# Kernel tuning notes

Hardware: AMD Instinct MI355X
Metric: run time of the kernel (lower is better)

The kernel has to match this reference:

```python
import jax, jax.numpy as jnp
import numpy as np
from functools import partial

H = 512          # hidden_size
H4 = H // 4      # goal hidden size
ENC = 8          # enc_steps
DEC = 12         # dec_steps
PRED = 2         # pred_dim (ETH)
B = 512          # batch


def _lin(k, i, o, s=0.05):
    kw, kb = jax.random.split(k)
    return jax.random.normal(kw, (i, o), jnp.float32) * s, jax.random.normal(kb, (o,), jnp.float32) * s


def setup_inputs() -> dict:
    key = jax.random.key(0)
    ks = jax.random.split(key, 32)
    d = {"inputs": jax.random.normal(ks[0], (B, ENC, 6), jnp.float32)}
    d["embed_w"], d["embed_b"] = _lin(ks[1], 6, H)
    d["reg_w"], d["reg_b"] = _lin(ks[2], H, PRED)
    d["ea_w"], d["ea_b"] = _lin(ks[3], H4, 1)
    d["da_w"], d["da_b"] = _lin(ks[4], H4, 1)
    d["e2g_w"], d["e2g_b"] = _lin(ks[5], H, H4)
    d["e2d_w"], d["e2d_b"] = _lin(ks[6], H, H)
    d["gh2i_w"], d["gh2i_b"] = _lin(ks[7], H4, H4)
    d["dh2i_w"], d["dh2i_b"] = _lin(ks[8], H, H)
    d["gh2t_w"], d["gh2t_b"] = _lin(ks[9], H4, H)
    d["g2e_w"], d["g2e_b"] = _lin(ks[10], H4, H4)
    d["g2d_w"], d["g2d_b"] = _lin(ks[11], H4, H4)
    d["enc_wih"], _ = _lin(ks[12], H + H4, 3 * H)
    d["enc_whh"], _ = _lin(ks[13], H, 3 * H)
    d["enc_bih"] = jax.random.normal(ks[14], (3 * H,), jnp.float32) * 0.05
    d["enc_bhh"] = jax.random.normal(ks[15], (3 * H,), jnp.float32) * 0.05
    d["goal_wih"], _ = _lin(ks[16], H4, 3 * H4)
    d["goal_whh"], _ = _lin(ks[17], H4, 3 * H4)
    d["goal_bih"] = jax.random.normal(ks[18], (3 * H4,), jnp.float32) * 0.05
    d["goal_bhh"] = jax.random.normal(ks[19], (3 * H4,), jnp.float32) * 0.05
    d["dec_wih"], _ = _lin(ks[20], H + H4, 3 * H)
    d["dec_whh"], _ = _lin(ks[21], H, 3 * H)
    d["dec_bih"] = jax.random.normal(ks[22], (3 * H,), jnp.float32) * 0.05
    d["dec_bhh"] = jax.random.normal(ks[23], (3 * H,), jnp.float32) * 0.05
    return d


def _gru(x, h, wih, whh, bih, bhh):
    gi = x @ wih + bih          # [B, 3H]
    gh = h @ whh + bhh
    ir, iz, inn = jnp.split(gi, 3, axis=-1)
    hr, hz, hn = jnp.split(gh, 3, axis=-1)
    r = jax.nn.sigmoid(ir + hr)
    z = jax.nn.sigmoid(iz + hz)
    n = jnp.tanh(inn + r * hn)
    return (1.0 - z) * n + z * h


def reference(inputs, embed_w, embed_b, reg_w, reg_b, ea_w, ea_b, da_w, da_b,
              e2g_w, e2g_b, e2d_w, e2d_b, gh2i_w, gh2i_b, dh2i_w, dh2i_b,
              gh2t_w, gh2t_b, g2e_w, g2e_b, g2d_w, g2d_b,
              enc_wih, enc_whh, enc_bih, enc_bhh,
              goal_wih, goal_whh, goal_bih, goal_bhh,
              dec_wih, dec_whh, dec_bih, dec_bhh):
    relu = jax.nn.relu
    b = inputs.shape[0]
    traj_input = relu(inputs @ embed_w + embed_b)           # [B, ENC, H]

    def sge(goal_hidden):
        def gstep(carry, _):
            gh, gi = carry
            gh = _gru(gi, gh, goal_wih, goal_whh, goal_bih, goal_bhh)
            gi = relu(gh @ gh2i_w + gh2i_b)
            return (gh, gi), gh
        gi0 = jnp.zeros((b, H4), traj_input.dtype)
        _, goals = jax.lax.scan(gstep, (goal_hidden, gi0), None, length=DEC)  # [DEC,B,H4]
        goal_traj = relu(goals @ gh2t_w + gh2t_b) @ reg_w + reg_b             # [DEC,B,PRED]
        goal_for_dec = relu(goals @ g2d_w + g2d_b)                            # [DEC,B,H4]
        gfe = relu(goals @ g2e_w + g2e_b).transpose(1, 0, 2)                  # [B,DEC,H4]
        logits = relu(jnp.tanh(gfe) @ ea_w + ea_b)[..., 0]                    # [B,DEC]
        attn = jax.nn.softmax(logits, axis=1)
        goal_for_enc = jnp.einsum('bt,bth->bh', attn, gfe)
        return goal_for_dec, goal_for_enc, goal_traj.transpose(1, 0, 2)

    def decoder(dec_hidden, gfd):
        gfd_b = gfd.transpose(1, 0, 2)  # [B,DEC,H4]
        steps = jnp.arange(DEC)
        def dstep(dh, t):
            mask = (steps >= t)[None, :, None]
            gdi = jnp.where(mask, gfd_b, 0.0)                      # zeros before t, faithful to torch
            logits = relu(jnp.tanh(gdi) @ da_w + da_b)[..., 0]     # [B,DEC]
            attn = jax.nn.softmax(logits, axis=1)
            ctx = jnp.einsum('bt,bth->bh', attn, gdi)
            ddi = relu(dh @ dh2i_w + dh2i_b)
            x = jnp.concatenate([ctx, ddi], axis=-1)
            dh = _gru(x, dh, dec_wih, dec_whh, dec_bih, dec_bhh)
            return dh, dh @ reg_w + reg_b
        _, traj = jax.lax.scan(dstep, dec_hidden, steps)           # [DEC,B,PRED]
        return traj.transpose(1, 0, 2)

    def estep(carry, x_t):
        teh, gfe = carry
        teh = _gru(jnp.concatenate([x_t, gfe], axis=1), teh,
                   enc_wih, enc_whh, enc_bih, enc_bhh)
        goal_hidden = relu(teh @ e2g_w + e2g_b)
        dec_hidden = relu(teh @ e2d_w + e2d_b)
        gfd, gfe, goal_traj = sge(goal_hidden)
        dec_traj = decoder(dec_hidden, gfd)
        return (teh, gfe), (goal_traj, dec_traj)

    teh0 = jnp.zeros((b, H), traj_input.dtype)
    gfe0 = jnp.zeros((b, H4), traj_input.dtype)
    _, (all_goal, all_dec) = jax.lax.scan(estep, (teh0, gfe0),
                                          traj_input.transpose(1, 0, 2))
    # [ENC,B,DEC,PRED] -> [B,ENC,DEC,PRED]
    return all_goal.transpose(1, 0, 2, 3), all_dec.transpose(1, 0, 2, 3)
```

## Files before the change

### kernel.cpp

```cpp
#include <hip/hip_runtime.h>


typedef unsigned short u16;
typedef __attribute__((ext_vector_type(8))) short bf16x8;
typedef __attribute__((ext_vector_type(4))) float f32x4;

static __device__ __forceinline__ float b2f(u16 u) {
  union { float f; unsigned int i; } x; x.i = ((unsigned int)u) << 16; return x.f;
}
static __device__ __forceinline__ u16 f2b(float f) {
  unsigned int u = __float_as_uint(f);
  unsigned int r = (u + 0x7FFFu + ((u >> 16) & 1u)) >> 16;
  return (u16)r;
}
static __device__ __forceinline__ float fsig(float x) {
  return __fdividef(1.f, 1.f + __expf(-x));
}
static __device__ __forceinline__ float ftanh(float x) {
  return 1.f - __fdividef(2.f, __expf(2.f * x) + 1.f);
}

struct TransArgs {
  const float* in[13];
  u16* out[13];
  int K[13], N[13], t0[13], nx[13];
};

__global__ __launch_bounds__(256) void transpose_all(TransArgs ta) {
  int bid = blockIdx.x;
  int i = 0;
  for (int k = 1; k < 13; k++) if (bid >= ta.t0[k]) i = k;
  const float* in = ta.in[i];
  u16* out = ta.out[i];
  int K = ta.K[i], N = ta.N[i];
  int local = bid - ta.t0[i];
  int nx = ta.nx[i];
  int tx = local % nx, ty = local / nx;
  __shared__ u16 tbuf[32][33];
  int n0 = tx * 32, k0 = ty * 32;
  int x = threadIdx.x & 31, y = threadIdx.x >> 5;
  for (int q = 0; q < 4; q++) tbuf[y + 8 * q][x] = f2b(in[(size_t)(k0 + y + 8 * q) * N + n0 + x]);
  __syncthreads();
  for (int q = 0; q < 4; q++) out[(size_t)(n0 + y + 8 * q) * K + k0 + x] = tbuf[x][y + 8 * q];
}

__global__ __launch_bounds__(256) void embed_kernel(const float* __restrict__ inp,
                                                    const float* __restrict__ w,
                                                    const float* __restrict__ bias,
                                                    u16* __restrict__ traj) {
  int t = blockIdx.x * 256 + threadIdx.x;
  int h = t & 511, b = (t >> 9) & 511, e = t >> 18;
  float acc = bias[h];
  for (int i = 0; i < 6; i++) acc += inp[(b * 8 + e) * 6 + i] * w[i * 512 + h];
  traj[((e * 512) + b) * 512 + h] = f2b(fmaxf(acc, 0.f));
}

struct GDesc {
  const u16* A; int lda;
  const u16* A2; int lda2; int asplit;
  const u16* W; int ldw;
  const float* bias;
  u16* Cb; int ldc;
  float* Cf;
  u16* Cb2; int ldc2; int route_n;
  int K; int relu; int nblk; int mblk;
};

__global__ __launch_bounds__(256) void gemm128(GDesc d0, GDesc d1) {
  GDesc d = (blockIdx.z == 0) ? d0 : d1;
  if ((int)blockIdx.x >= d.nblk || (int)blockIdx.y >= d.mblk) return;
  __shared__ u16 As[128][72];
  __shared__ u16 Bs[128][72];
  int tid = threadIdx.x;
  int m0 = blockIdx.y * 128, n0 = blockIdx.x * 128;
  int lane = tid & 63, wave = tid >> 6;
  int wr = wave >> 1, wc = wave & 1;
  int mrow = lane & 15, kq = (lane >> 4) * 8;
  int srow = tid >> 3, scol = (tid & 7) * 8;
  f32x4 acc[4][4] = {};

  for (int k0 = 0; k0 < d.K; k0 += 64) {
    const u16* Asrc; int Alda, kk;
    if (k0 < d.asplit) { Asrc = d.A; Alda = d.lda; kk = k0; }
    else               { Asrc = d.A2; Alda = d.lda2; kk = k0 - d.asplit; }
    __syncthreads();
#pragma unroll
    for (int p = 0; p < 4; p++) {
      int r = srow + p * 32;
      *(uint4*)&As[r][scol] = *(const uint4*)&Asrc[(size_t)(m0 + r) * Alda + kk + scol];
      *(uint4*)&Bs[r][scol] = *(const uint4*)&d.W[(size_t)(n0 + r) * d.ldw + k0 + scol];
    }
    __syncthreads();
#pragma unroll
    for (int ks = 0; ks < 2; ks++) {
      bf16x8 af[4], bf[4];
#pragma unroll
      for (int i = 0; i < 4; i++) {
        af[i] = *(const bf16x8*)&As[wr * 64 + i * 16 + mrow][ks * 32 + kq];
        bf[i] = *(const bf16x8*)&Bs[wc * 64 + i * 16 + mrow][ks * 32 + kq];
      }
#pragma unroll
      for (int i = 0; i < 4; i++)
#pragma unroll
        for (int j = 0; j < 4; j++)
          acc[i][j] = __builtin_amdgcn_mfma_f32_16x16x32_bf16(af[i], bf[j], acc[i][j], 0, 0, 0);
    }
  }
  int col = lane & 15, rq = (lane >> 4) * 4;
#pragma unroll
  for (int j = 0; j < 4; j++) {
    int n = n0 + wc * 64 + j * 16 + col;
    float bv = d.bias ? d.bias[n] : 0.f;
    bool r2 = (n >= d.route_n);
    u16* cb = r2 ? d.Cb2 : d.Cb;
    int ldc = r2 ? d.ldc2 : d.ldc;
    int nn = r2 ? n - d.route_n : n;
#pragma unroll
    for (int i = 0; i < 4; i++)
#pragma unroll
      for (int r = 0; r < 4; r++) {
        int m = m0 + wr * 64 + i * 16 + rq + r;
        float v = acc[i][j][r] + bv;
        if (d.relu) v = fmaxf(v, 0.f);
        cb[(size_t)m * ldc + nn] = f2b(v);
        if (d.Cf) d.Cf[(size_t)m * d.ldc + n] = v;
      }
  }
}

__global__ __launch_bounds__(256) void head_reg(const u16* __restrict__ goals,
                                                const u16* __restrict__ w_t,
                                                const float* __restrict__ wb,
                                                const float* __restrict__ rw,
                                                const float* __restrict__ rb,
                                                float* __restrict__ out) {
  int tid = threadIdx.x;
  int lane = tid & 63, wave = tid >> 6;
  int rbase = (blockIdx.x * 4 + wave) * 64;
  int mrow = lane & 15, kq = (lane >> 4) * 8;
  int col = lane & 15, rq4 = (lane >> 4) * 4;
  bf16x8 a[4][4];
#pragma unroll
  for (int q = 0; q < 4; q++)
#pragma unroll
    for (int ks = 0; ks < 4; ks++)
      a[q][ks] = *(const bf16x8*)&goals[(size_t)(rbase + q * 16 + mrow) * 128 + ks * 32 + kq];
  float pr0[4][4] = {}, pr1[4][4] = {};
  for (int j = 0; j < 32; j++) {
    bf16x8 b[4];
#pragma unroll
    for (int ks = 0; ks < 4; ks++)
      b[ks] = *(const bf16x8*)&w_t[(size_t)(j * 16 + mrow) * 128 + ks * 32 + kq];
    f32x4 acc[4] = {};
#pragma unroll
    for (int ks = 0; ks < 4; ks++)
#pragma unroll
      for (int q = 0; q < 4; q++)
        acc[q] = __builtin_amdgcn_mfma_f32_16x16x32_bf16(a[q][ks], b[ks], acc[q], 0, 0, 0);
    int n = j * 16 + col;
    float bv = wb[n];
    float rw0 = rw[n * 2], rw1 = rw[n * 2 + 1];
#pragma unroll
    for (int q = 0; q < 4; q++)
#pragma unroll
      for (int r = 0; r < 4; r++) {
        float v = fmaxf(acc[q][r] + bv, 0.f);
        pr0[q][r] += v * rw0;
        pr1[q][r] += v * rw1;
      }
  }
#pragma unroll
  for (int q = 0; q < 4; q++)
#pragma unroll
    for (int r = 0; r < 4; r++)
#pragma unroll
      for (int o = 1; o < 16; o <<= 1) {
        pr0[q][r] += __shfl_xor(pr0[q][r], o);
        pr1[q][r] += __shfl_xor(pr1[q][r], o);
      }
  if (col == 0) {
#pragma unroll
    for (int q = 0; q < 4; q++)
#pragma unroll
      for (int r = 0; r < 4; r++) {
        int m = rbase + q * 16 + rq4 + r;
        int e = m / 6144; int rem = m - e * 6144;
        int t = rem >> 9; int b = rem & 511;
        float* o = out + ((size_t)(b * 8 + e) * 12 + t) * 2;
        o[0] = pr0[q][r] + rb[0];
        o[1] = pr1[q][r] + rb[1];
      }
  }
}

__global__ __launch_bounds__(1024) void gru_dh2i_reg(const u16* __restrict__ gi,
                                                     const u16* __restrict__ gh,
                                                     float* __restrict__ hf,
                                                     u16* __restrict__ hb,
                                                     const u16* __restrict__ w_t,
                                                     const float* __restrict__ wb,
                                                     u16* __restrict__ ddi,
                                                     const float* __restrict__ rw,
                                                     const float* __restrict__ rb,
                                                     float* __restrict__ out, int td) {
  __shared__ u16 dhs[16][520];
  __shared__ u16 dds[16][520];
  int tid = threadIdx.x;
  int lane = tid & 63, wave = tid >> 6;
  int r0 = blockIdx.x * 16;
  {
    int r = r0 + wave;
    int j8 = lane * 8;
    size_t base = (size_t)r * 1536 + j8;
    uint4 ir4 = *(const uint4*)&gi[base];
    uint4 iz4 = *(const uint4*)&gi[base + 512];
    uint4 in4 = *(const uint4*)&gi[base + 1024];
    uint4 hr4 = *(const uint4*)&gh[base];
    uint4 hz4 = *(const uint4*)&gh[base + 512];
    uint4 hn4 = *(const uint4*)&gh[base + 1024];
    const u16* irp = (const u16*)&ir4; const u16* izp = (const u16*)&iz4;
    const u16* inp = (const u16*)&in4; const u16* hrp = (const u16*)&hr4;
    const u16* hzp = (const u16*)&hz4; const u16* hnp = (const u16*)&hn4;
    size_t hoff = (size_t)r * 512 + j8;
    float hv[8];
    *(float4*)&hv[0] = *(const float4*)&hf[hoff];
    *(float4*)&hv[4] = *(const float4*)&hf[hoff + 4];
    u16 hbv[8];
    float p0 = 0.f, p1 = 0.f;
    for (int j = 0; j < 8; j++) {
      float rr = fsig(b2f(irp[j]) + b2f(hrp[j]));
      float zz = fsig(b2f(izp[j]) + b2f(hzp[j]));
      float nn = ftanh(b2f(inp[j]) + rr * b2f(hnp[j]));
      float ho = (1.f - zz) * nn + zz * hv[j];
      hv[j] = ho; hbv[j] = f2b(ho);
      p0 += ho * rw[(j8 + j) * 2];
      p1 += ho * rw[(j8 + j) * 2 + 1];
    }
    *(float4*)&hf[hoff] = *(const float4*)&hv[0];
    *(float4*)&hf[hoff + 4] = *(const float4*)&hv[4];
    *(uint4*)&hb[hoff] = *(const uint4*)&hbv[0];
    *(uint4*)&dhs[wave][j8] = *(const uint4*)&hbv[0];
    for (int o = 32; o; o >>= 1) { p0 += __shfl_down(p0, o); p1 += __shfl_down(p1, o); }
    if (lane == 0) {
      int e = r >> 9, b = r & 511;
      size_t off = ((size_t)(b * 8 + e) * 12 + td) * 2;
      out[off] = p0 + rb[0];
      out[off + 1] = p1 + rb[1];
    }
  }
  __syncthreads();
  int mrow = lane & 15, kq = (lane >> 4) * 8, rq4 = (lane >> 4) * 4;
#pragma unroll
  for (int q = 0; q < 2; q++) {
    int n0 = (wave * 2 + q) * 16;
    f32x4 acc = {};
#pragma unroll
    for (int ks = 0; ks < 16; ks++) {
      bf16x8 a = *(const bf16x8*)&dhs[mrow][ks * 32 + kq];
      bf16x8 bfr = *(const bf16x8*)&w_t[(size_t)(n0 + mrow) * 512 + ks * 32 + kq];
      acc = __builtin_amdgcn_mfma_f32_16x16x32_bf16(a, bfr, acc, 0, 0, 0);
    }
    float bv = wb[n0 + mrow];
#pragma unroll
    for (int x = 0; x < 4; x++)
      dds[rq4 + x][n0 + mrow] = f2b(fmaxf(acc[x] + bv, 0.f));
  }
  __syncthreads();
  int rr = tid >> 6, c8 = (tid & 63) * 8;
  *(uint4*)&ddi[(size_t)(r0 + rr) * 512 + c8] = *(const uint4*)&dds[rr][c8];
}

__global__ __launch_bounds__(1024) void goal_mega(const u16* __restrict__ gi_g,
                                                  const u16* __restrict__ gh_g,
                                                  float* __restrict__ teh_f,
                                                  u16* __restrict__ teh_out,
                                                  const u16* __restrict__ e2g_t,
                                                  const float* __restrict__ e2g_b,
                                                  const u16* __restrict__ wih_t,
                                                  const u16* __restrict__ whh_t,
                                                  const float* __restrict__ bih,
                                                  const float* __restrict__ bhh,
                                                  const u16* __restrict__ g2i_t,
                                                  const float* __restrict__ g2i_b,
                                                  const u16* __restrict__ g2e_t,
                                                  const float* __restrict__ g2e_b,
                                                  const float* __restrict__ eaw,
                                                  const float* __restrict__ eab,
                                                  u16* __restrict__ goals,
                                                  u16* __restrict__ gfe_out) {
  __shared__ float ghf[16][128];
  __shared__ u16   ghb[16][136];
  __shared__ u16   gib[16][136];
  __shared__ float gi3[16][388];
  __shared__ float gh3[16][388];
  __shared__ u16   gfe_l[12][16][128];
  __shared__ u16   tehb[16][520];
  int tid = threadIdx.x;
  int r0 = blockIdx.x * 16;
  int lane = tid & 63, wave = tid >> 6;
  int mrow = lane & 15, kq = (lane >> 4) * 8;
  int rq4 = (lane >> 4) * 4;

  bool isI = (wave < 8);
  int tbase = isI ? wave : wave - 8;
  bf16x8 Bf[3][4];
  float  bias1[3];
  int    n0s[3];
#pragma unroll
  for (int i = 0; i < 3; i++) {
    int n0 = (tbase + 8 * i) * 16;
    n0s[i] = n0;
    const u16* Wt = isI ? wih_t : whh_t;
#pragma unroll
    for (int ks = 0; ks < 4; ks++)
      Bf[i][ks] = *(const bf16x8*)&Wt[(n0 + mrow) * 128 + ks * 32 + kq];
    bias1[i] = (isI ? bih : bhh)[n0 + mrow];
  }
  bf16x8 Gf[4];
  float bias3;
  {
    const u16* W3 = isI ? g2i_t : g2e_t;
    const float* B3 = isI ? g2i_b : g2e_b;
    int n0 = (wave & 7) * 16;
#pragma unroll
    for (int ks = 0; ks < 4; ks++)
      Gf[ks] = *(const bf16x8*)&W3[(n0 + mrow) * 128 + ks * 32 + kq];
    bias3 = B3[n0 + mrow];
  }

  {
    u16* gz = &gib[0][0];
    for (int idx = tid; idx < 16 * 136; idx += 1024) gz[idx] = 0;
  }

  {
    int r = wave;
    int j8 = lane * 8;
    int grow = r0 + r;
    size_t base = (size_t)grow * 1536 + j8;
    uint4 ir4 = *(const uint4*)&gi_g[base];
    uint4 iz4 = *(const uint4*)&gi_g[base + 512];
    uint4 in4 = *(const uint4*)&gi_g[base + 1024];
    uint4 hr4 = *(const uint4*)&gh_g[base];
    uint4 hz4 = *(const uint4*)&gh_g[base + 512];
    uint4 hn4 = *(const uint4*)&gh_g[base + 1024];
    const u16* irp = (const u16*)&ir4; const u16* izp = (const u16*)&iz4;
    const u16* inp = (const u16*)&in4; const u16* hrp = (const u16*)&hr4;
    const u16* hzp = (const u16*)&hz4; const u16* hnp = (const u16*)&hn4;
    size_t hoff = (size_t)grow * 512 + j8;
    float hv[8];
    *(float4*)&hv[0] = *(const float4*)&teh_f[hoff];
    *(float4*)&hv[4] = *(const float4*)&teh_f[hoff + 4];
    u16 hbv[8];
    for (int j = 0; j < 8; j++) {
      float rr = fsig(b2f(irp[j]) + b2f(hrp[j]));
      float zz = fsig(b2f(izp[j]) + b2f(hzp[j]));
      float nn = ftanh(b2f(inp[j]) + rr * b2f(hnp[j]));
      float ho = (1.f - zz) * nn + zz * hv[j];
      hv[j] = ho; hbv[j] = f2b(ho);
    }
    *(float4*)&teh_f[hoff] = *(const float4*)&hv[0];
    *(float4*)&teh_f[hoff + 4] = *(const float4*)&hv[4];
    *(uint4*)&teh_out[hoff] = *(const uint4*)&hbv[0];
    *(uint4*)&tehb[r][j8] = *(const uint4*)&hbv[0];
  }
  __syncthreads();

  if (wave < 8) {
    int n0 = wave * 16;
    f32x4 acc = {};
#pragma unroll
    for (int ks = 0; ks < 16; ks++) {
      bf16x8 a = *(const bf16x8*)&tehb[mrow][ks * 32 + kq];
      bf16x8 b = *(const bf16x8*)&e2g_t[(size_t)(n0 + mrow) * 512 + ks * 32 + kq];
      acc = __builtin_amdgcn_mfma_f32_16x16x32_bf16(a, b, acc, 0, 0, 0);
    }
    int n = n0 + mrow;
    float bv = e2g_b[n];
#pragma unroll
    for (int r = 0; r < 4; r++) {
      float v = fmaxf(acc[r] + bv, 0.f);
      int m = rq4 + r;
      ghf[m][n] = v;
      ghb[m][n] = f2b(v);
    }
  }
  __syncthreads();

  for (int t = 0; t < 12; t++) {
    bf16x8 ag[4];
#pragma unroll
    for (int ks = 0; ks < 4; ks++)
      ag[ks] = isI ? *(const bf16x8*)&gib[mrow][ks * 32 + kq]
                   : *(const bf16x8*)&ghb[mrow][ks * 32 + kq];
    float* G = isI ? &gi3[0][0] : &gh3[0][0];
#pragma unroll
    for (int i = 0; i < 3; i++) {
      f32x4 acc = {};
#pragma unroll
      for (int ks = 0; ks < 4; ks++)
        acc = __builtin_amdgcn_mfma_f32_16x16x32_bf16(ag[ks], Bf[i][ks], acc, 0, 0, 0);
      int n = n0s[i] + mrow;
#pragma unroll
      for (int r = 0; r < 4; r++)
        G[(rq4 + r) * 388 + n] = acc[r] + bias1[i];
    }
    __syncthreads();
    for (int idx = tid; idx < 2048; idx += 1024) {
      int m = idx >> 7, j = idx & 127;
      float rr = fsig(gi3[m][j] + gh3[m][j]);
      float zz = fsig(gi3[m][128 + j] + gh3[m][128 + j]);
      float nn = ftanh(gi3[m][256 + j] + rr * gh3[m][256 + j]);
      float h = ghf[m][j];
      float ho = (1.f - zz) * nn + zz * h;
      ghf[m][j] = ho;
      ghb[m][j] = f2b(ho);
    }
    __syncthreads();
    if (wave < 4) {
      int idx = wave * 64 + lane;
      int row = idx >> 4, c8 = (idx & 15) * 8;
      uint4 v = *(const uint4*)&ghb[row][c8];
      *(uint4*)&goals[(size_t)(t * 512 + r0 + row) * 128 + c8] = v;
    }
    {
      f32x4 acc = {};
#pragma unroll
      for (int ks = 0; ks < 4; ks++) {
        bf16x8 a = *(const bf16x8*)&ghb[mrow][ks * 32 + kq];
        acc = __builtin_amdgcn_mfma_f32_16x16x32_bf16(a, Gf[ks], acc, 0, 0, 0);
      }
      int n = (wave & 7) * 16 + mrow;
      if (isI) {
#pragma unroll
        for (int r = 0; r < 4; r++)
          gib[rq4 + r][n] = f2b(fmaxf(acc[r] + bias3, 0.f));
      } else {
#pragma unroll
        for (int r = 0; r < 4; r++)
          gfe_l[t][rq4 + r][n] = f2b(fmaxf(acc[r] + bias3, 0.f));
      }
    }
    __syncthreads();
  }

  {
    int m = wave;
    float w0 = eaw[lane], w1 = eaw[lane + 64];
    float eb = eab[0];
    float v0[12], v1[12], lg[12];
#pragma unroll
    for (int t = 0; t < 12; t++) {
      float a = b2f(gfe_l[t][m][lane]);
      float c = b2f(gfe_l[t][m][lane + 64]);
      v0[t] = a; v1[t] = c;
      float p = ftanh(a) * w0 + ftanh(c) * w1;
      for (int o = 32; o; o >>= 1) p += __shfl_xor(p, o);
      lg[t] = fmaxf(p + eb, 0.f);
    }
    float mx = lg[0];
#pragma unroll
    for (int t = 1; t < 12; t++) mx = fmaxf(mx, lg[t]);
    float s = 0.f;
#pragma unroll
    for (int t = 0; t < 12; t++) { lg[t] = __expf(lg[t] - mx); s += lg[t]; }
    float inv = __fdividef(1.f, s);
    float c0 = 0.f, c1 = 0.f;
#pragma unroll
    for (int t = 0; t < 12; t++) { c0 += lg[t] * inv * v0[t]; c1 += lg[t] * inv * v1[t]; }
    gfe_out[(r0 + m) * 128 + lane] = f2b(c0);
    gfe_out[(r0 + m) * 128 + lane + 64] = f2b(c1);
  }
}

__global__ __launch_bounds__(256) void attn_ctx_all(const u16* __restrict__ gfd,
                                                    const float* __restrict__ daw,
                                                    const float* __restrict__ dab,
                                                    u16* __restrict__ xctx) {
  int row = (blockIdx.x * 256 + threadIdx.x) >> 6;
  int lane = threadIdx.x & 63;
  int e = row >> 9, b = row & 511;
  float w0 = daw[lane], w1 = daw[lane + 64];
  float bias = dab[0];
  float v0[12], v1[12], lg[12];
#pragma unroll
  for (int s = 0; s < 12; s++) {
    size_t o = ((size_t)(e * 12 + s) * 512 + b) * 128;
    float a = b2f(gfd[o + lane]);
    float c = b2f(gfd[o + 64 + lane]);
    v0[s] = a; v1[s] = c;
    float p = ftanh(a) * w0 + ftanh(c) * w1;
    for (int o2 = 32; o2; o2 >>= 1) p += __shfl_xor(p, o2);
    lg[s] = fmaxf(p + bias, 0.f);
  }
  float base = fmaxf(bias, 0.f);
  float m = base;
#pragma unroll
  for (int s = 0; s < 12; s++) m = fmaxf(m, lg[s]);
  float eb = __expf(base - m);
  float el[12];
#pragma unroll
  for (int s = 0; s < 12; s++) el[s] = __expf(lg[s] - m);
  float S0 = 0.f, S1 = 0.f, sufE = 0.f;
#pragma unroll
  for (int td = 11; td >= 0; td--) {
    sufE += el[td];
    S0 += el[td] * v0[td];
    S1 += el[td] * v1[td];
    float inv = __fdividef(1.f, (float)td * eb + sufE);
    size_t o = ((size_t)td * 4096 + row) * 128;
    xctx[o + lane] = f2b(S0 * inv);
    xctx[o + lane + 64] = f2b(S1 * inv);
  }
}

extern "C" void kernel_launch(void* const* d_in, const int* in_sizes, int n_in,
                              void* d_out, int out_size, void* d_ws, size_t ws_size,
                              hipStream_t stream) {
  const float* inp      = (const float*)d_in[0];
  const float* embed_w  = (const float*)d_in[1];
  const float* embed_b  = (const float*)d_in[2];
  const float* reg_w    = (const float*)d_in[3];
  const float* reg_b    = (const float*)d_in[4];
  const float* ea_w     = (const float*)d_in[5];
  const float* ea_b     = (const float*)d_in[6];
  const float* da_w     = (const float*)d_in[7];
  const float* da_b     = (const float*)d_in[8];
  const float* e2g_w    = (const float*)d_in[9];
  const float* e2g_b    = (const float*)d_in[10];
  const float* e2d_w    = (const float*)d_in[11];
  const float* e2d_b    = (const float*)d_in[12];
  const float* gh2i_w   = (const float*)d_in[13];
  const float* gh2i_b   = (const float*)d_in[14];
  const float* dh2i_w   = (const float*)d_in[15];
  const float* dh2i_b   = (const float*)d_in[16];
  const float* gh2t_w   = (const float*)d_in[17];
  const float* gh2t_b   = (const float*)d_in[18];
  const float* g2e_w    = (const float*)d_in[19];
  const float* g2e_b    = (const float*)d_in[20];
  const float* g2d_w    = (const float*)d_in[21];
  const float* g2d_b    = (const float*)d_in[22];
  const float* enc_wih  = (const float*)d_in[23];
  const float* enc_whh  = (const float*)d_in[24];
  const float* enc_bih  = (const float*)d_in[25];
  const float* enc_bhh  = (const float*)d_in[26];
  const float* goal_wih = (const float*)d_in[27];
  const float* goal_whh = (const float*)d_in[28];
  const float* goal_bih = (const float*)d_in[29];
  const float* goal_bhh = (const float*)d_in[30];
  const float* dec_wih  = (const float*)d_in[31];
  const float* dec_whh  = (const float*)d_in[32];
  const float* dec_bih  = (const float*)d_in[33];
  const float* dec_bhh  = (const float*)d_in[34];

  char* ws = (char*)d_ws;
  size_t off = 0;
  auto alloc = [&](size_t bytes) -> char* {
    char* p = ws + off; off += (bytes + 255) & ~(size_t)255; return p;
  };
  const size_t TSZ = 512 * 512;
  float* teh_f    = (float*)alloc(TSZ * 4);
  u16*   teh_hist = (u16*)  alloc(9 * TSZ * 2);
  u16*   gfe_buf  = (u16*)  alloc(512 * 128 * 2);
  size_t zero_bytes = off;
  u16*   traj     = (u16*)  alloc((size_t)8 * TSZ * 2);
  u16*   goals_all= (u16*)  alloc((size_t)8 * 6144 * 128 * 2);
  u16*   gfd      = (u16*)  alloc((size_t)49152 * 128 * 2);
  u16*   xctx     = (u16*)  alloc((size_t)12 * 4096 * 128 * 2);
  float* dh_f     = (float*)alloc((size_t)4096 * 512 * 4);
  u16*   dh_b     = (u16*)  alloc((size_t)4096 * 512 * 2);
  u16*   ddi      = (u16*)  alloc((size_t)4096 * 512 * 2);
  u16*   giD      = (u16*)  alloc((size_t)4096 * 1536 * 2);
  u16*   ghD      = (u16*)  alloc((size_t)4096 * 1536 * 2);
  u16*   giE = giD, *ghE = ghD;
  u16* enc_wih_t  = (u16*)alloc((size_t)1536 * 640 * 2);
  u16* enc_whh_t  = (u16*)alloc((size_t)1536 * 512 * 2);
  u16* dec_wih_t  = (u16*)alloc((size_t)1536 * 640 * 2);
  u16* dec_whh_t  = (u16*)alloc((size_t)1536 * 512 * 2);
  u16* e2g_t      = (u16*)alloc(128 * 512 * 2);
  u16* e2d_t      = (u16*)alloc(512 * 512 * 2);
  u16* dh2i_t     = (u16*)alloc(512 * 512 * 2);
  u16* head_t     = (u16*)alloc(640 * 128 * 2);
  u16* g2e_t      = (u16*)alloc(128 * 128 * 2);
  u16* goal_wih_t = (u16*)alloc(384 * 128 * 2);
  u16* goal_whh_t = (u16*)alloc(384 * 128 * 2);
  u16* gh2i_t     = (u16*)alloc(128 * 128 * 2);
  if (off > ws_size) return;

  float* out_goal = (float*)d_out;
  float* out_dec  = out_goal + (size_t)512 * 8 * 12 * 2;

  hipMemsetAsync(teh_f, 0, zero_bytes, stream);

  TransArgs ta;
  int ntile = 0, ti = 0;
  auto push = [&](const float* in, u16* out, int K, int N) {
    ta.in[ti] = in; ta.out[ti] = out; ta.K[ti] = K; ta.N[ti] = N;
    ta.t0[ti] = ntile; ta.nx[ti] = N / 32;
    ntile += (K / 32) * (N / 32); ti++;
  };
  push(enc_wih, enc_wih_t, 640, 1536);
  push(enc_whh, enc_whh_t, 512, 1536);
  push(dec_wih, dec_wih_t, 640, 1536);
  push(dec_whh, dec_whh_t, 512, 1536);
  push(e2g_w, e2g_t, 512, 128);
  push(e2d_w, e2d_t, 512, 512);
  push(dh2i_w, dh2i_t, 512, 512);
  push(gh2t_w, head_t, 128, 512);
  push(g2d_w, head_t + 512 * 128, 128, 128);
  push(g2e_w, g2e_t, 128, 128);
  push(goal_wih, goal_wih_t, 128, 384);
  push(goal_whh, goal_whh_t, 128, 384);
  push(gh2i_w, gh2i_t, 128, 128);
  transpose_all<<<ntile, 256, 0, stream>>>(ta);

  embed_kernel<<<8192, 256, 0, stream>>>(inp, embed_w, embed_b, traj);

  const int FAR = 1 << 30;

  for (int e = 0; e < 8; ++e) {
    GDesc dgi{traj + (size_t)e * TSZ, 512, gfe_buf, 128, 512,
              enc_wih_t, 640, enc_bih, giE, 1536, nullptr,
              nullptr, 0, FAR, 640, 0, 12, 4};
    GDesc dgh{teh_hist + (size_t)e * TSZ, 512, nullptr, 0, FAR,
              enc_whh_t, 512, enc_bhh, ghE, 1536, nullptr,
              nullptr, 0, FAR, 512, 0, 12, 4};
    gemm128<<<dim3(12, 4, 2), 256, 0, stream>>>(dgi, dgh);
    goal_mega<<<32, 1024, 0, stream>>>(giE, ghE, teh_f, teh_hist + (size_t)(e + 1) * TSZ,
                                       e2g_t, e2g_b,
                                       goal_wih_t, goal_whh_t, goal_bih, goal_bhh,
                                       gh2i_t, gh2i_b, g2e_t, g2e_b, ea_w, ea_b,
                                       goals_all + (size_t)e * 6144 * 128, gfe_buf);
  }

  {
    head_reg<<<192, 256, 0, stream>>>(goals_all, head_t, gh2t_b, reg_w, reg_b, out_goal);
    GDesc dg2d{goals_all, 128, nullptr, 0, FAR,
               head_t + 512 * 128, 128, g2d_b, gfd, 128, nullptr,
               nullptr, 0, FAR, 128, 1, 1, 384};
    GDesc de2d{teh_hist + TSZ, 512, nullptr, 0, FAR,
               e2d_t, 512, e2d_b, dh_b, 512, dh_f,
               nullptr, 0, FAR, 512, 1, 4, 32};
    gemm128<<<dim3(4, 384, 2), 256, 0, stream>>>(dg2d, de2d);
    attn_ctx_all<<<1024, 256, 0, stream>>>(gfd, da_w, da_b, xctx);
    GDesc dd0{dh_b, 512, nullptr, 0, FAR,
              dh2i_t, 512, dh2i_b, ddi, 512, nullptr,
              nullptr, 0, FAR, 512, 1, 4, 32};
    gemm128<<<dim3(4, 32, 1), 256, 0, stream>>>(dd0, dd0);
  }

  for (int td = 0; td < 12; ++td) {
    GDesc dgi{xctx + (size_t)td * 4096 * 128, 128, ddi, 512, 128,
              dec_wih_t, 640, dec_bih, giD, 1536, nullptr,
              nullptr, 0, FAR, 640, 0, 12, 32};
    GDesc dgh{dh_b, 512, nullptr, 0, FAR,
              dec_whh_t, 512, dec_bhh, ghD, 1536, nullptr,
              nullptr, 0, FAR, 512, 0, 12, 32};
    gemm128<<<dim3(12, 32, 2), 256, 0, stream>>>(dgi, dgh);
    gru_dh2i_reg<<<256, 1024, 0, stream>>>(giD, ghD, dh_f, dh_b, dh2i_t, dh2i_b, ddi,
                                           reg_w, reg_b, out_dec, td);
  }
}
```

Before: 1.277 ms.

## Fuse goal GRU gates in registers and halve goal_mega block to 512 threads

The goal GRU recurrence in goal_mega is restructured so each of 8 waves computes both the input and hidden projections for the same 16 output columns. The gate math then runs directly on the MFMA accumulators in registers, with the hidden state also kept in registers. This removes the fp32 gi3/gh3/ghf shared-memory staging and one barrier per step, and ghb is double-buffered to avoid a read/write race. The goals output is written straight from registers, the g2i/g2e projections are computed by the same waves, and the block shrinks from 1024 to 512 threads. In exchange each wave holds twice as many weight fragments in registers and does more serial MFMA work, with fewer waves available to hide latency.

```diff
diff --git a/kernel.cpp b/kernel.cpp
--- a/kernel.cpp
+++ b/kernel.cpp
@@ -270,71 +270,70 @@
   *(uint4*)&ddi[(size_t)(r0 + rr) * 512 + c8] = *(const uint4*)&dds[rr][c8];
 }
 
-__global__ __launch_bounds__(1024) void goal_mega(const u16* __restrict__ gi_g,
-                                                  const u16* __restrict__ gh_g,
-                                                  float* __restrict__ teh_f,
-                                                  u16* __restrict__ teh_out,
-                                                  const u16* __restrict__ e2g_t,
-                                                  const float* __restrict__ e2g_b,
-                                                  const u16* __restrict__ wih_t,
-                                                  const u16* __restrict__ whh_t,
-                                                  const float* __restrict__ bih,
-                                                  const float* __restrict__ bhh,
-                                                  const u16* __restrict__ g2i_t,
-                                                  const float* __restrict__ g2i_b,
-                                                  const u16* __restrict__ g2e_t,
-                                                  const float* __restrict__ g2e_b,
-                                                  const float* __restrict__ eaw,
-                                                  const float* __restrict__ eab,
-                                                  u16* __restrict__ goals,
-                                                  u16* __restrict__ gfe_out) {
-  __shared__ float ghf[16][128];
-  __shared__ u16   ghb[16][136];
-  __shared__ u16   gib[16][136];
-  __shared__ float gi3[16][388];
-  __shared__ float gh3[16][388];
-  __shared__ u16   gfe_l[12][16][128];
-  __shared__ u16   tehb[16][520];
+__global__ __launch_bounds__(512) void goal_mega(const u16* __restrict__ gi_g,
+                                                 const u16* __restrict__ gh_g,
+                                                 float* __restrict__ teh_f,
+                                                 u16* __restrict__ teh_out,
+                                                 const u16* __restrict__ e2g_t,
+                                                 const float* __restrict__ e2g_b,
+                                                 const u16* __restrict__ wih_t,
+                                                 const u16* __restrict__ whh_t,
+                                                 const float* __restrict__ bih,
+                                                 const float* __restrict__ bhh,
+                                                 const u16* __restrict__ g2i_t,
+                                                 const float* __restrict__ g2i_b,
+                                                 const u16* __restrict__ g2e_t,
+                                                 const float* __restrict__ g2e_b,
+                                                 const float* __restrict__ eaw,
+                                                 const float* __restrict__ eab,
+                                                 u16* __restrict__ goals,
+                                                 u16* __restrict__ gfe_out) {
+  __shared__ u16 ghb[2][16][136];
+  __shared__ u16 gib[16][136];
+  __shared__ u16 gfe_l[12][16][128];
+  __shared__ u16 tehb[16][520];
   int tid = threadIdx.x;
   int r0 = blockIdx.x * 16;
   int lane = tid & 63, wave = tid >> 6;
   int mrow = lane & 15, kq = (lane >> 4) * 8;
   int rq4 = (lane >> 4) * 4;
-
-  bool isI = (wave < 8);
-  int tbase = isI ? wave : wave - 8;
-  bf16x8 Bf[3][4];
-  float  bias1[3];
-  int    n0s[3];
+  int col = lane & 15;
+  int ncol = wave * 16 + col;
+
+  bf16x8 BfI[3][4], BfH[3][4];
+  float bI[3], bH[3];
 #pragma unroll
   for (int i = 0; i < 3; i++) {
-    int n0 = (tbase + 8 * i) * 16;
-    n0s[i] = n0;
-    const u16* Wt = isI ? wih_t : whh_t;
-#pragma unroll
-    for (int ks = 0; ks < 4; ks++)
-      Bf[i][ks] = *(const bf16x8*)&Wt[(n0 + mrow) * 128 + ks * 32 + kq];
-    bias1[i] = (isI ? bih : bhh)[n0 + mrow];
-  }
-  bf16x8 Gf[4];
-  float bias3;
+    int n0 = (wave + 8 * i) * 16;
+#pragma unroll
+    for (int ks = 0; ks < 4; ks++) {
+      BfI[i][ks] = *(const bf16x8*)&wih_t[(n0 + mrow) * 128 + ks * 32 + kq];
+      BfH[i][ks] = *(const bf16x8*)&whh_t[(n0 + mrow) * 128 + ks * 32 + kq];
+    }
+    bI[i] = bih[n0 + col];
+    bH[i] = bhh[n0 + col];
+  }
+  bf16x8 GfI[4], GfE[4];
+  float bGi, bGe;
   {
-    const u16* W3 = isI ? g2i_t : g2e_t;
-    const float* B3 = isI ? g2i_b : g2e_b;
-    int n0 = (wave & 7) * 16;
-#pragma unroll
-    for (int ks = 0; ks < 4; ks++)
-      Gf[ks] = *(const bf16x8*)&W3[(n0 + mrow) * 128 + ks * 32 + kq];
-    bias3 = B3[n0 + mrow];
+    int n0 = wave * 16;
+#pragma unroll
+    for (int ks = 0; ks < 4; ks++) {
+      GfI[ks] = *(const bf16x8*)&g2i_t[(n0 + mrow) * 128 + ks * 32 + kq];
+      GfE[ks] = *(const bf16x8*)&g2e_t[(n0 + mrow) * 128 + ks * 32 + kq];
+    }
+    bGi = g2i_b[n0 + col];
+    bGe = g2e_b[n0 + col];
   }
 
   {
     u16* gz = &gib[0][0];
-    for (int idx = tid; idx < 16 * 136; idx += 1024) gz[idx] = 0;
-  }
-
-  {
-    int r = wave;
+    for (int idx = tid; idx < 16 * 136; idx += 512) gz[idx] = 0;
+  }
+
+#pragma unroll
+  for (int rep = 0; rep < 2; rep++) {
+    int r = wave + 8 * rep;
     int j8 = lane * 8;
     int grow = r0 + r;
     size_t base = (size_t)grow * 1536 + j8;
@@ -366,86 +365,77 @@
   }
   __syncthreads();
 
-  if (wave < 8) {
-    int n0 = wave * 16;
+  f32x4 hreg;
+  {
     f32x4 acc = {};
 #pragma unroll
     for (int ks = 0; ks < 16; ks++) {
       bf16x8 a = *(const bf16x8*)&tehb[mrow][ks * 32 + kq];
-      bf16x8 b = *(const bf16x8*)&e2g_t[(size_t)(n0 + mrow) * 512 + ks * 32 + kq];
+      bf16x8 b = *(const bf16x8*)&e2g_t[(size_t)(wave * 16 + mrow) * 512 + ks * 32 + kq];
       acc = __builtin_amdgcn_mfma_f32_16x16x32_bf16(a, b, acc, 0, 0, 0);
     }
-    int n = n0 + mrow;
-    float bv = e2g_b[n];
+    float bv = e2g_b[ncol];
 #pragma unroll
     for (int r = 0; r < 4; r++) {
       float v = fmaxf(acc[r] + bv, 0.f);
-      int m = rq4 + r;
-      ghf[m][n] = v;
-      ghb[m][n] = f2b(v);
+      hreg[r] = v;
+      ghb[0][rq4 + r][ncol] = f2b(v);
     }
   }
   __syncthreads();
 
   for (int t = 0; t < 12; t++) {
-    bf16x8 ag[4];
+    int p = t & 1;
+    bf16x8 agi[4], agh[4];
+#pragma unroll
+    for (int ks = 0; ks < 4; ks++) {
+      agi[ks] = *(const bf16x8*)&gib[mrow][ks * 32 + kq];
+      agh[ks] = *(const bf16x8*)&ghb[p][mrow][ks * 32 + kq];
+    }
+    f32x4 gI[3], gH[3];
+#pragma unroll
+    for (int i = 0; i < 3; i++) {
+      f32x4 a1 = {}, a2 = {};
+#pragma unroll
+      for (int ks = 0; ks < 4; ks++) {
+        a1 = __builtin_amdgcn_mfma_f32_16x16x32_bf16(agi[ks], BfI[i][ks], a1, 0, 0, 0);
+        a2 = __builtin_amdgcn_mfma_f32_16x16x32_bf16(agh[ks], BfH[i][ks], a2, 0, 0, 0);
+      }
+      gI[i] = a1; gH[i] = a2;
+    }
+#pragma unroll
+    for (int r = 0; r < 4; r++) {
+      float rr = fsig(gI[0][r] + bI[0] + gH[0][r] + bH[0]);
+      float zz = fsig(gI[1][r] + bI[1] + gH[1][r] + bH[1]);
+      float nn = ftanh(gI[2][r] + bI[2] + rr * (gH[2][r] + bH[2]));
+      float ho = (1.f - zz) * nn + zz * hreg[r];
+      hreg[r] = ho;
+      u16 hb = f2b(ho);
+      ghb[1 - p][rq4 + r][ncol] = hb;
+      goals[(size_t)(t * 512 + r0 + rq4 + r) * 128 + ncol] = hb;
+    }
+    __syncthreads();
+    bf16x8 ah[4];
 #pragma unroll
     for (int ks = 0; ks < 4; ks++)
-      ag[ks] = isI ? *(const bf16x8*)&gib[mrow][ks * 32 + kq]
-                   : *(const bf16x8*)&ghb[mrow][ks * 32 + kq];
-    float* G = isI ? &gi3[0][0] : &gh3[0][0];
-#pragma unroll
-    for (int i = 0; i < 3; i++) {
-      f32x4 acc = {};
-#pragma unroll
-      for (int ks = 0; ks < 4; ks++)
-        acc = __builtin_amdgcn_mfma_f32_16x16x32_bf16(ag[ks], Bf[i][ks], acc, 0, 0, 0);
-      int n = n0s[i] + mrow;
-#pragma unroll
-      for (int r = 0; r < 4; r++)
-        G[(rq4 + r) * 388 + n] = acc[r] + bias1[i];
+      ah[ks] = *(const bf16x8*)&ghb[1 - p][mrow][ks * 32 + kq];
+    f32x4 ai = {}, ae = {};
+#pragma unroll
+    for (int ks = 0; ks < 4; ks++) {
+      ai = __builtin_amdgcn_mfma_f32_16x16x32_bf16(ah[ks], GfI[ks], ai, 0, 0, 0);
+      ae = __builtin_amdgcn_mfma_f32_16x16x32_bf16(ah[ks], GfE[ks], ae, 0, 0, 0);
+    }
+#pragma unroll
+    for (int r = 0; r < 4; r++) {
+      gib[rq4 + r][ncol] = f2b(fmaxf(ai[r] + bGi, 0.f));
+      gfe_l[t][rq4 + r][ncol] = f2b(fmaxf(ae[r] + bGe, 0.f));
     }
     __syncthreads();
-    for (int idx = tid; idx < 2048; idx += 1024) {
-      int m = idx >> 7, j = idx & 127;
-      float rr = fsig(gi3[m][j] + gh3[m][j]);
-      float zz = fsig(gi3[m][128 + j] + gh3[m][128 + j]);
-      float nn = ftanh(gi3[m][256 + j] + rr * gh3[m][256 + j]);
-      float h = ghf[m][j];
-      float ho = (1.f - zz) * nn + zz * h;
-      ghf[m][j] = ho;
-      ghb[m][j] = f2b(ho);
-    }
-    __syncthreads();
-    if (wave < 4) {
-      int idx = wave * 64 + lane;
-      int row = idx >> 4, c8 = (idx & 15) * 8;
-      uint4 v = *(const uint4*)&ghb[row][c8];
-      *(uint4*)&goals[(size_t)(t * 512 + r0 + row) * 128 + c8] = v;
-    }
-    {
-      f32x4 acc = {};
-#pragma unroll
-      for (int ks = 0; ks < 4; ks++) {
-        bf16x8 a = *(const bf16x8*)&ghb[mrow][ks * 32 + kq];
-        acc = __builtin_amdgcn_mfma_f32_16x16x32_bf16(a, Gf[ks], acc, 0, 0, 0);
-      }
-      int n = (wave & 7) * 16 + mrow;
-      if (isI) {
-#pragma unroll
-        for (int r = 0; r < 4; r++)
-          gib[rq4 + r][n] = f2b(fmaxf(acc[r] + bias3, 0.f));
-      } else {
-#pragma unroll
-        for (int r = 0; r < 4; r++)
-          gfe_l[t][rq4 + r][n] = f2b(fmaxf(acc[r] + bias3, 0.f));
-      }
-    }
-    __syncthreads();
-  }
-
-  {
-    int m = wave;
+  }
+
+#pragma unroll
+  for (int rep = 0; rep < 2; rep++) {
+    int m = wave + 8 * rep;
     float w0 = eaw[lane], w1 = eaw[lane + 64];
     float eb = eab[0];
     float v0[12], v1[12], lg[12];
@@ -454,9 +444,9 @@
       float a = b2f(gfe_l[t][m][lane]);
       float c = b2f(gfe_l[t][m][lane + 64]);
       v0[t] = a; v1[t] = c;
-      float p = ftanh(a) * w0 + ftanh(c) * w1;
-      for (int o = 32; o; o >>= 1) p += __shfl_xor(p, o);
-      lg[t] = fmaxf(p + eb, 0.f);
+      float pv = ftanh(a) * w0 + ftanh(c) * w1;
+      for (int o = 32; o; o >>= 1) pv += __shfl_xor(pv, o);
+      lg[t] = fmaxf(pv + eb, 0.f);
     }
     float mx = lg[0];
 #pragma unroll
@@ -626,11 +616,11 @@
               enc_whh_t, 512, enc_bhh, ghE, 1536, nullptr,
               nullptr, 0, FAR, 512, 0, 12, 4};
     gemm128<<<dim3(12, 4, 2), 256, 0, stream>>>(dgi, dgh);
-    goal_mega<<<32, 1024, 0, stream>>>(giE, ghE, teh_f, teh_hist + (size_t)(e + 1) * TSZ,
-                                       e2g_t, e2g_b,
-                                       goal_wih_t, goal_whh_t, goal_bih, goal_bhh,
-                                       gh2i_t, gh2i_b, g2e_t, g2e_b, ea_w, ea_b,
-                                       goals_all + (size_t)e * 6144 * 128, gfe_buf);
+    goal_mega<<<32, 512, 0, stream>>>(giE, ghE, teh_f, teh_hist + (size_t)(e + 1) * TSZ,
+                                      e2g_t, e2g_b,
+                                      goal_wih_t, goal_whh_t, goal_bih, goal_bhh,
+                                      gh2i_t, gh2i_b, g2e_t, g2e_b, ea_w, ea_b,
+                                      goals_all + (size_t)e * 6144 * 128, gfe_buf);
   }
 
   {
```

Result: faster. 1.247 ms (-2.3%).
